# Optimization experiments

Measured on AMD Instinct MI355X. Metric: run time of the kernel, lower is better.

Reference implementation:

```python
import jax, jax.numpy as jnp
import numpy as np

B, P, M, D = 16, 1024, 4, 64

def setup_inputs() -> dict:
    key = jax.random.key(0)
    k1, k2 = jax.random.split(key)
    values = jax.random.normal(k1, (B, P, D), dtype=jnp.float32)
    preattention = jax.random.normal(k2, (B, P, M), dtype=jnp.float32)
    mask = jnp.ones((B, P, 1), dtype=jnp.float32)
    return {"values": values, "preattention": preattention, "mask": mask}

def reference(values, preattention, mask):
    # values: [B,P,d], preattention: [B,P,m], mask: [B,P,1]
    # running cumulative max over the sequence for numerical stability
    cmax = jax.lax.cummax(preattention, axis=1)              # [B,P,m]
    # D[b,p,q,m] = exp(pre[b,q,m] - cmax[b,p,m]) for q <= p, else 0
    d = jnp.exp(preattention[:, None, :, :] - cmax[:, :, None, :])  # [B,P,Q,m]
    causal = jnp.tril(jnp.ones((preattention.shape[1], preattention.shape[1]), dtype=bool))
    d = jnp.where(causal[None, :, :, None], d, jnp.float32(0.0))
    e = d.sum(axis=2)                                        # [B,P,m]
    out = jnp.einsum('BPQm,BQd->BPmd', d, values) / e[:, :, :, None]
    out = out * mask[:, :, :, None]                          # [B,P,1,1] broadcast
    return out
```

## Files before the change

kernel.cpp:

```cpp
#include <hip/hip_runtime.h>
#include <math.h>

#define BATCH 16
#define SEQ 1024
#define MH 4
#define DIM 64
#define NCHUNK 8
#define CHUNK 128
#define WAVES 8
#define WSEG 16
#define THREADS (WAVES * 64)

__global__ __launch_bounds__(THREADS)
void teedam_kernel(const float* __restrict__ values,
                   const float* __restrict__ pre,
                   const float* __restrict__ mask,
                   float* __restrict__ out) {
    const int blk  = blockIdx.x;
    const int c    = blk & (NCHUNK - 1);
    const int bm   = blk >> 3;
    const int m    = bm & (MH - 1);
    const int b    = bm >> 2;

    const int tid  = threadIdx.x;
    const int w    = tid >> 6;
    const int lane = tid & 63;

    const int bP = b * SEQ;
    const int p0 = c * CHUNK;

    __shared__ float lds_red[WAVES];
    __shared__ float lds_Sb[WAVES];
    __shared__ float lds_Sc[WAVES];
    __shared__ float lds_Ab[WAVES][DIM];
    __shared__ float lds_Ac[WAVES][DIM];

    const int npos = p0 + CHUNK;
    float gmax = -INFINITY;
    for (int p = tid; p < npos; p += THREADS)
        gmax = fmaxf(gmax, pre[(size_t)(bP + p) * MH + m]);
    #pragma unroll
    for (int off = 32; off > 0; off >>= 1)
        gmax = fmaxf(gmax, __shfl_xor(gmax, off, 64));
    if (lane == 0) lds_red[w] = gmax;
    __syncthreads();
    float G = lds_red[0];
    #pragma unroll
    for (int j = 1; j < WAVES; ++j) G = fmaxf(G, lds_red[j]);

    float Sb0 = 0.f, Sb1 = 0.f, Ab0 = 0.f, Ab1 = 0.f;
    for (int t = 0; t < c; ++t) {
        const int g  = w + t * 8;
        const int q0 = g * 16;
        float pre_b = (lane < 16) ? pre[(size_t)(bP + q0 + lane) * MH + m] : 0.f;
        const float* vb = values + (size_t)(bP + q0) * DIM + lane;
        #pragma unroll
        for (int i = 0; i < 16; i += 2) {
            float w0 = __expf(__shfl(pre_b, i, 64) - G);
            float w1 = __expf(__shfl(pre_b, i + 1, 64) - G);
            Sb0 += w0;
            Sb1 += w1;
            Ab0 = fmaf(w0, vb[(size_t)i * DIM], Ab0);
            Ab1 = fmaf(w1, vb[(size_t)(i + 1) * DIM], Ab1);
        }
    }
    if (lane == 0) lds_Sb[w] = Sb0 + Sb1;
    lds_Ab[w][lane] = Ab0 + Ab1;

    const int q0c = p0 + w * WSEG;
    float pre_c  = (lane < 16) ? pre[(size_t)(bP + q0c + lane) * MH + m] : 0.f;
    float mask_c = (lane < 16) ? mask[bP + q0c + lane] : 0.f;
    const float* vc = values + (size_t)(bP + q0c) * DIM + lane;
    float Sc = 0.f, Ac = 0.f;
    #pragma unroll
    for (int i = 0; i < WSEG; ++i) {
        float wq = __expf(__shfl(pre_c, i, 64) - G);
        Sc += wq;
        Ac = fmaf(wq, vc[(size_t)i * DIM], Ac);
    }
    if (lane == 0) lds_Sc[w] = Sc;
    lds_Ac[w][lane] = Ac;
    __syncthreads();

    float S = 0.f, A = 0.f;
    #pragma unroll
    for (int j = 0; j < WAVES; ++j) { S += lds_Sb[j]; A += lds_Ab[j][lane]; }
    for (int j = 0; j < w; ++j)     { S += lds_Sc[j]; A += lds_Ac[j][lane]; }

    float* op = out + ((size_t)(bP + q0c) * MH + m) * DIM + lane;
    #pragma unroll
    for (int i = 0; i < WSEG; ++i) {
        float wq = __expf(__shfl(pre_c, i, 64) - G);
        float vv = vc[(size_t)i * DIM];
        S += wq;
        A = fmaf(wq, vv, A);
        float mk = __shfl(mask_c, i, 64);
        op[(size_t)i * MH * DIM] = A * (mk * __builtin_amdgcn_rcpf(S));
    }
}

extern "C" void kernel_launch(void* const* d_in, const int* in_sizes, int n_in,
                              void* d_out, int out_size, void* d_ws, size_t ws_size,
                              hipStream_t stream) {
    const float* values = (const float*)d_in[0];
    const float* pre    = (const float*)d_in[1];
    const float* mask   = (const float*)d_in[2];
    float*       out    = (float*)d_out;

    dim3 grid(BATCH * MH * NCHUNK);
    dim3 block(THREADS);
    hipLaunchKernelGGL(teedam_kernel, grid, block, 0, stream,
                       values, pre, mask, out);
}
```

Baseline: 18.12 us.

## Split into per-chunk partials kernel and prefix-combining finalize kernel

Replaces the single kernel, in which chunk c re-read and re-weighted every earlier chunk, with two kernels. The first computes per-chunk partials (local max, weighted sum, weighted value accumulator) into the workspace. The second rescales and combines the partials of earlier chunks, log-sum-exp style, before the in-chunk scan. This removes the quadratic redundant reads of values across chunks, at the cost of an extra kernel launch and a workspace round trip.

```diff
diff --git a/kernel.cpp b/kernel.cpp
--- a/kernel.cpp
+++ b/kernel.cpp
@@ -7,20 +7,69 @@
 #define DIM 64
 #define NCHUNK 8
 #define CHUNK 128
-#define WAVES 8
-#define WSEG 16
-#define THREADS (WAVES * 64)
+#define WS_STRIDE 68
 
-__global__ __launch_bounds__(THREADS)
-void teedam_kernel(const float* __restrict__ values,
-                   const float* __restrict__ pre,
-                   const float* __restrict__ mask,
-                   float* __restrict__ out) {
-    const int blk  = blockIdx.x;
-    const int c    = blk & (NCHUNK - 1);
-    const int bm   = blk >> 3;
-    const int m    = bm & (MH - 1);
-    const int b    = bm >> 2;
+__global__ __launch_bounds__(256)
+void teedam_partials(const float* __restrict__ values,
+                     const float* __restrict__ pre,
+                     float* __restrict__ ws) {
+    const int blk = blockIdx.x;
+    const int c   = blk & (NCHUNK - 1);
+    const int bm  = blk >> 3;
+    const int m   = bm & (MH - 1);
+    const int b   = bm >> 2;
+
+    const int tid  = threadIdx.x;
+    const int w    = tid >> 6;
+    const int lane = tid & 63;
+
+    const int bP = b * SEQ;
+    const int q0 = c * CHUNK + w * 32;
+
+    __shared__ float sM[4], sS[4], sA[4][DIM];
+
+    float pre_l = (lane < 32) ? pre[(size_t)(bP + q0 + lane) * MH + m] : -INFINITY;
+
+    float mx = pre_l;
+    #pragma unroll
+    for (int off = 16; off > 0; off >>= 1)
+        mx = fmaxf(mx, __shfl_xor(mx, off, 64));
+    if (lane == 0) sM[w] = mx;
+    __syncthreads();
+    const float Mc = fmaxf(fmaxf(sM[0], sM[1]), fmaxf(sM[2], sM[3]));
+
+    const float* vb = values + (size_t)(bP + q0) * DIM + lane;
+    float S = 0.f, A = 0.f;
+    #pragma unroll
+    for (int i = 0; i < 32; ++i) {
+        float wq = __expf(__shfl(pre_l, i, 64) - Mc);
+        S += wq;
+        A = fmaf(wq, vb[(size_t)i * DIM], A);
+    }
+    if (lane == 0) sS[w] = S;
+    sA[w][lane] = A;
+    __syncthreads();
+
+    if (w == 0) {
+        float St = sS[0] + sS[1] + sS[2] + sS[3];
+        float At = sA[0][lane] + sA[1][lane] + sA[2][lane] + sA[3][lane];
+        float* wp = ws + (size_t)blk * WS_STRIDE;
+        if (lane == 0) { wp[0] = Mc; wp[1] = St; }
+        wp[2 + lane] = At;
+    }
+}
+
+__global__ __launch_bounds__(512)
+void teedam_finalize(const float* __restrict__ values,
+                     const float* __restrict__ pre,
+                     const float* __restrict__ mask,
+                     const float* __restrict__ ws,
+                     float* __restrict__ out) {
+    const int blk = blockIdx.x;
+    const int c   = blk & (NCHUNK - 1);
+    const int bm  = blk >> 3;
+    const int m   = bm & (MH - 1);
+    const int b   = bm >> 2;
 
     const int tid  = threadIdx.x;
     const int w    = tid >> 6;
@@ -29,67 +78,42 @@
     const int bP = b * SEQ;
     const int p0 = c * CHUNK;
 
-    __shared__ float lds_red[WAVES];
-    __shared__ float lds_Sb[WAVES];
-    __shared__ float lds_Sc[WAVES];
-    __shared__ float lds_Ab[WAVES][DIM];
-    __shared__ float lds_Ac[WAVES][DIM];
+    __shared__ float sS[8], sA[8][DIM];
 
-    const int npos = p0 + CHUNK;
-    float gmax = -INFINITY;
-    for (int p = tid; p < npos; p += THREADS)
-        gmax = fmaxf(gmax, pre[(size_t)(bP + p) * MH + m]);
-    #pragma unroll
-    for (int off = 32; off > 0; off >>= 1)
-        gmax = fmaxf(gmax, __shfl_xor(gmax, off, 64));
-    if (lane == 0) lds_red[w] = gmax;
-    __syncthreads();
-    float G = lds_red[0];
-    #pragma unroll
-    for (int j = 1; j < WAVES; ++j) G = fmaxf(G, lds_red[j]);
+    const float* wsbase = ws + (size_t)(bm * NCHUNK) * WS_STRIDE;
+    float G = -INFINITY;
+    for (int j = 0; j <= c; ++j) G = fmaxf(G, wsbase[(size_t)j * WS_STRIDE]);
 
-    float Sb0 = 0.f, Sb1 = 0.f, Ab0 = 0.f, Ab1 = 0.f;
-    for (int t = 0; t < c; ++t) {
-        const int g  = w + t * 8;
-        const int q0 = g * 16;
-        float pre_b = (lane < 16) ? pre[(size_t)(bP + q0 + lane) * MH + m] : 0.f;
-        const float* vb = values + (size_t)(bP + q0) * DIM + lane;
-        #pragma unroll
-        for (int i = 0; i < 16; i += 2) {
-            float w0 = __expf(__shfl(pre_b, i, 64) - G);
-            float w1 = __expf(__shfl(pre_b, i + 1, 64) - G);
-            Sb0 += w0;
-            Sb1 += w1;
-            Ab0 = fmaf(w0, vb[(size_t)i * DIM], Ab0);
-            Ab1 = fmaf(w1, vb[(size_t)(i + 1) * DIM], Ab1);
-        }
+    float Spre = 0.f, Apre = 0.f;
+    for (int j = 0; j < c; ++j) {
+        const float* wj = wsbase + (size_t)j * WS_STRIDE;
+        float ej = __expf(wj[0] - G);
+        Spre = fmaf(wj[1], ej, Spre);
+        Apre = fmaf(wj[2 + lane], ej, Apre);
     }
-    if (lane == 0) lds_Sb[w] = Sb0 + Sb1;
-    lds_Ab[w][lane] = Ab0 + Ab1;
 
-    const int q0c = p0 + w * WSEG;
+    const int q0c = p0 + w * 16;
     float pre_c  = (lane < 16) ? pre[(size_t)(bP + q0c + lane) * MH + m] : 0.f;
     float mask_c = (lane < 16) ? mask[bP + q0c + lane] : 0.f;
     const float* vc = values + (size_t)(bP + q0c) * DIM + lane;
+
     float Sc = 0.f, Ac = 0.f;
     #pragma unroll
-    for (int i = 0; i < WSEG; ++i) {
+    for (int i = 0; i < 16; ++i) {
         float wq = __expf(__shfl(pre_c, i, 64) - G);
         Sc += wq;
         Ac = fmaf(wq, vc[(size_t)i * DIM], Ac);
     }
-    if (lane == 0) lds_Sc[w] = Sc;
-    lds_Ac[w][lane] = Ac;
+    if (lane == 0) sS[w] = Sc;
+    sA[w][lane] = Ac;
     __syncthreads();
 
-    float S = 0.f, A = 0.f;
-    #pragma unroll
-    for (int j = 0; j < WAVES; ++j) { S += lds_Sb[j]; A += lds_Ab[j][lane]; }
-    for (int j = 0; j < w; ++j)     { S += lds_Sc[j]; A += lds_Ac[j][lane]; }
+    float S = Spre, A = Apre;
+    for (int j = 0; j < w; ++j) { S += sS[j]; A += sA[j][lane]; }
 
     float* op = out + ((size_t)(bP + q0c) * MH + m) * DIM + lane;
     #pragma unroll
-    for (int i = 0; i < WSEG; ++i) {
+    for (int i = 0; i < 16; ++i) {
         float wq = __expf(__shfl(pre_c, i, 64) - G);
         float vv = vc[(size_t)i * DIM];
         S += wq;
@@ -106,9 +130,11 @@
     const float* pre    = (const float*)d_in[1];
     const float* mask   = (const float*)d_in[2];
     float*       out    = (float*)d_out;
+    float*       ws     = (float*)d_ws;
 
     dim3 grid(BATCH * MH * NCHUNK);
-    dim3 block(THREADS);
-    hipLaunchKernelGGL(teedam_kernel, grid, block, 0, stream,
-                       values, pre, mask, out);
+    hipLaunchKernelGGL(teedam_partials, grid, dim3(256), 0, stream,
+                       values, pre, ws);
+    hipLaunchKernelGGL(teedam_finalize, grid, dim3(512), 0, stream,
+                       values, pre, mask, ws, out);
 }
```

New measurement: 19.53 us. +7.8%, slower.
